# Performance work log

Hardware: AMD Instinct MI355X
Metric: run time of the kernel (lower is better)

The kernel has to match this reference:

```python
import jax, jax.numpy as jnp
import numpy as np

B, S, D, H, M = 4, 512, 768, 12, 4
DFF = 4 * D
HD = D // H
EPS = 1e-6  # timm/jvp_layers LayerNorm eps
SCALE = HD ** -0.5


def _ln(x, g, b):
    mu = jnp.mean(x, axis=-1, keepdims=True)
    var = jnp.mean((x - mu) ** 2, axis=-1, keepdims=True)
    return (x - mu) * jax.lax.rsqrt(var + EPS) * g + b


def _block(x, g1, b1, Wqkv, Wproj, bproj, g2, b2, W1, bf1, W2, bf2):
    # pre-norm attention
    h = _ln(x, g1, b1)
    qkv = h @ Wqkv                       # [B,S,3D]
    q, k, v = jnp.split(qkv, 3, axis=-1)
    q = q.reshape(B, S, H, HD)
    k = k.reshape(B, S, H, HD)
    v = v.reshape(B, S, H, HD)
    scores = jnp.einsum('bqhd,bkhd->bhqk', q, k) * SCALE
    attn = jax.nn.softmax(scores, axis=-1)
    o = jnp.einsum('bhqk,bkhd->bqhd', attn, v).reshape(B, S, D)
    x = x + o @ Wproj + bproj
    # pre-norm MLP
    h2 = _ln(x, g2, b2)
    mlp = jax.nn.gelu(h2 @ W1 + bf1, approximate=False) @ W2 + bf2
    return x + mlp


def setup_inputs() -> dict:
    key = jax.random.key(0)
    ks = jax.random.split(key, 8)
    w = 0.02
    return {
        'x': jax.random.normal(ks[0], (B, S, D), jnp.float32),
        'x_tangent': jax.random.normal(ks[1], (B, M, S, D), jnp.float32),
        'g1': jnp.ones((D,), jnp.float32),
        'b1': jnp.zeros((D,), jnp.float32),
        'Wqkv': jax.random.normal(ks[2], (D, 3 * D), jnp.float32) * w,
        'Wproj': jax.random.normal(ks[3], (D, D), jnp.float32) * w,
        'bproj': jnp.zeros((D,), jnp.float32),
        'g2': jnp.ones((D,), jnp.float32),
        'b2': jnp.zeros((D,), jnp.float32),
        'W1': jax.random.normal(ks[4], (D, DFF), jnp.float32) * w,
        'bf1': jnp.zeros((DFF,), jnp.float32),
        'W2': jax.random.normal(ks[5], (DFF, D), jnp.float32) * w,
        'bf2': jnp.zeros((D,), jnp.float32),
    }


def reference(x, x_tangent, g1, b1, Wqkv, Wproj, bproj, g2, b2, W1, bf1, W2, bf2):
    f = lambda xx: _block(xx, g1, b1, Wqkv, Wproj, bproj, g2, b2, W1, bf1, W2, bf2)
    # linearize once: primal + efficient JVP for all M tangent directions
    out, jvp_fn = jax.linearize(f, x)
    out_tangent = jax.vmap(jvp_fn, in_axes=1, out_axes=1)(x_tangent)  # [B,M,S,D]
    return out, out_tangent
```

## Files before the change

### kernel.cpp

```cpp
#include <hip/hip_runtime.h>
#include <math.h>

constexpr int B_ = 4, S_ = 512, D_ = 768, H_ = 12, M_ = 4, DFF_ = 3072, HD_ = 64;
constexpr float EPS_ = 1e-6f;
constexpr float SCALE_ = 0.125f;
constexpr int BS_ = B_ * S_;
constexpr int BH_ = B_ * H_;
constexpr long long BSD_ = (long long)BS_ * D_;
constexpr long long BS3D_ = (long long)BS_ * 3 * D_;
constexpr long long ATT_ = (long long)BH_ * S_ * S_;
constexpr long long BSF_ = (long long)BS_ * DFF_;

typedef __attribute__((ext_vector_type(8))) short bf16x8;
typedef __attribute__((ext_vector_type(4))) float f32x4;

__device__ __forceinline__ ushort f2bf(float f) {
    uint32_t u = __float_as_uint(f);
    u += 0x7FFF + ((u >> 16) & 1);
    return (ushort)(u >> 16);
}
__device__ __forceinline__ float bf2f(ushort u) {
    return __uint_as_float((uint32_t)u << 16);
}

__device__ __forceinline__ void gll16(const ushort* g, ushort* l) {
    __builtin_amdgcn_global_load_lds((const __attribute__((address_space(1))) void*)g,
                                     (__attribute__((address_space(3))) void*)l, 16, 0, 0);
}

template <int N> __device__ __forceinline__ void waitcnt_vm() {
    if constexpr (N == 0) asm volatile("s_waitcnt vmcnt(0)" ::: "memory");
    else if constexpr (N == 4) asm volatile("s_waitcnt vmcnt(4)" ::: "memory");
    else if constexpr (N == 6) asm volatile("s_waitcnt vmcnt(6)" ::: "memory");
    else if constexpr (N == 8) asm volatile("s_waitcnt vmcnt(8)" ::: "memory");
    else static_assert(N == 0 || N == 4 || N == 6 || N == 8, "add literal");
}

__device__ __forceinline__ void waitcnt_lgkm0() {
    asm volatile("s_waitcnt lgkmcnt(0)" ::: "memory");
    __builtin_amdgcn_sched_barrier(0);
}

__device__ __forceinline__ int xcd_swz(int flat, int nwg) {
    int q = nwg >> 3, r = nwg & 7;
    int x = flat & 7, pos = flat >> 3;
    int base = (x < r) ? x * (q + 1) : r * (q + 1) + (x - r) * q;
    return base + pos;
}

__device__ __forceinline__ size_t stroff(int rg, int c, int Nc) {
    int m = rg >> 11;
    int b = (rg >> 9) & (B_ - 1);
    int s = rg & (S_ - 1);
    return ((size_t)((b * M_ + m) * S_ + s)) * Nc + c;
}

__device__ __forceinline__ float block_sum(float v) {
    __shared__ float red[4];
    int tid = threadIdx.x;
#pragma unroll
    for (int off = 32; off > 0; off >>= 1) v += __shfl_down(v, off, 64);
    __syncthreads();
    if ((tid & 63) == 0) red[tid >> 6] = v;
    __syncthreads();
    return red[0] + red[1] + red[2] + red[3];
}

__device__ __forceinline__ float block_max(float v) {
    __shared__ float red[4];
    int tid = threadIdx.x;
#pragma unroll
    for (int off = 32; off > 0; off >>= 1) v = fmaxf(v, __shfl_down(v, off, 64));
    __syncthreads();
    if ((tid & 63) == 0) red[tid >> 6] = v;
    __syncthreads();
    return fmaxf(fmaxf(red[0], red[1]), fmaxf(red[2], red[3]));
}

__global__ __launch_bounds__(256) void transpose_f2b(const float* __restrict__ W,
                                                     ushort* __restrict__ WT,
                                                     int K, int N) {
    __shared__ float t[32][33];
    int n0 = blockIdx.x * 32, k0 = blockIdx.y * 32;
    int tx = threadIdx.x & 31, ty = threadIdx.x >> 5;
#pragma unroll
    for (int i = 0; i < 4; i++)
        t[ty + i * 8][tx] = W[(size_t)(k0 + ty + i * 8) * N + n0 + tx];
    __syncthreads();
#pragma unroll
    for (int i = 0; i < 4; i++)
        WT[(size_t)(n0 + ty + i * 8) * K + k0 + tx] = f2bf(t[tx][ty + i * 8]);
}

__global__ __launch_bounds__(256) void transpose_v(const ushort* __restrict__ src0,
                                                   ushort* __restrict__ Vt0,
                                                   ushort* __restrict__ dVt4) {
    int z = blockIdx.z;
    int m = z / BH_, bh = z % BH_;
    const ushort* qkvb = src0 + (size_t)m * BS3D_;
    ushort* Vt = (m == 0) ? Vt0 : dVt4 + (size_t)(m - 1) * BSD_;
    int b = bh / H_, hh = bh - b * H_;
    int s0 = blockIdx.x * 32, d0 = blockIdx.y * 32;
    __shared__ ushort t[32][33];
    int tx = threadIdx.x & 31, ty = threadIdx.x >> 5;
#pragma unroll
    for (int i = 0; i < 4; i++)
        t[ty + i * 8][tx] = qkvb[(size_t)(b * S_ + s0 + ty + i * 8) * 3 * D_ + 2 * D_ + hh * HD_ + d0 + tx];
    __syncthreads();
#pragma unroll
    for (int i = 0; i < 4; i++)
        Vt[(size_t)bh * HD_ * S_ + (size_t)(d0 + ty + i * 8) * S_ + s0 + tx] = t[tx][ty + i * 8];
}

__global__ __launch_bounds__(256) void ln_fwd(const float* __restrict__ xf,
                                              const ushort* __restrict__ xb,
                                              const float* __restrict__ g,
                                              const float* __restrict__ bta,
                                              ushort* __restrict__ xhat,
                                              ushort* __restrict__ h,
                                              float* __restrict__ rstd) {
    int row = blockIdx.x;
    size_t base = (size_t)row * D_;
    int tid = threadIdx.x;
    float v[3];
    float s = 0.f;
#pragma unroll
    for (int i = 0; i < 3; i++) {
        int c = tid + i * 256;
        v[i] = xf ? xf[base + c] : bf2f(xb[base + c]);
        s += v[i];
    }
    s = block_sum(s);
    float mu = s * (1.0f / D_);
    float vs = 0.f;
#pragma unroll
    for (int i = 0; i < 3; i++) { float c = v[i] - mu; vs += c * c; }
    vs = block_sum(vs);
    float rs = rsqrtf(vs * (1.0f / D_) + EPS_);
#pragma unroll
    for (int i = 0; i < 3; i++) {
        int c = tid + i * 256;
        float xh = (v[i] - mu) * rs;
        xhat[base + c] = f2bf(xh);
        h[base + c] = f2bf(xh * g[c] + bta[c]);
    }
    if (tid == 0) rstd[row] = rs;
}

__global__ __launch_bounds__(256) void ln_jvp(const float* __restrict__ tf,
                                              const ushort* __restrict__ tb, int mode,
                                              const ushort* __restrict__ xhat,
                                              const float* __restrict__ rstd,
                                              const float* __restrict__ g,
                                              ushort* __restrict__ dh,
                                              ushort* __restrict__ xtb) {
    int rg = blockIdx.x;
    int r = rg & (BS_ - 1);
    size_t pbase = (size_t)r * D_;
    int tid = threadIdx.x;
    float tv[3], xh[3];
    float s1 = 0.f, s2 = 0.f;
    size_t tbase;
    if (mode == 0) {
        int m = rg >> 11;
        int b = r >> 9, s = r & (S_ - 1);
        tbase = ((size_t)((b * M_ + m) * S_ + s)) * D_;
    } else {
        tbase = (size_t)rg * D_;
    }
#pragma unroll
    for (int i = 0; i < 3; i++) {
        int c = tid + i * 256;
        tv[i] = (mode == 0) ? tf[tbase + c] : bf2f(tb[tbase + c]);
        xh[i] = bf2f(xhat[pbase + c]);
        s1 += tv[i];
        s2 += tv[i] * xh[i];
    }
    s1 = block_sum(s1);
    s2 = block_sum(s2);
    float mt = s1 * (1.0f / D_);
    float mx = s2 * (1.0f / D_);
    float rs = rstd[r];
#pragma unroll
    for (int i = 0; i < 3; i++) {
        int c = tid + i * 256;
        dh[(size_t)rg * D_ + c] = f2bf(g[c] * rs * (tv[i] - mt - xh[i] * mx));
        if (mode == 0 && xtb) xtb[(size_t)rg * D_ + c] = f2bf(tv[i]);
    }
}

template <int BM, int BN, int EPI>
__global__ __launch_bounds__(256) void gemm_mfma(const ushort* __restrict__ A,
                                                 const ushort* __restrict__ BT,
                                                 const float* __restrict__ bias,
                                                 const float* __restrict__ resf,
                                                 const ushort* __restrict__ resb,
                                                 const ushort* __restrict__ resb2,
                                                 float* __restrict__ Cf,
                                                 float* __restrict__ Cf2,
                                                 ushort* __restrict__ Cb,
                                                 ushort* __restrict__ aux,
                                                 int Nc, int Kd) {
    constexpr int FI = BM / 32, FJ = BN / 32;
    constexpr int LA = BM / 32, LB = BN / 32, L = LA + LB;
    __shared__ ushort As[2][BM * 64];
    __shared__ ushort Bs[2][BN * 64];
    int tid = threadIdx.x;
    int wave = tid >> 6, lane = tid & 63;
    int wr = wave >> 1, wc = wave & 1;
    int gx = gridDim.x, nwg = gx * gridDim.y;
    int work = xcd_swz(blockIdx.x + blockIdx.y * gx, nwg);
    int band = work / (8 * gx);
    int wi = work - band * (8 * gx);
    int row0 = (band * 8 + (wi & 7)) * BM;
    int col0 = (wi >> 3) * BN;

    int srow = lane >> 3;
    int skel = ((lane & 7) ^ (lane >> 3)) * 8;
    const ushort* Ag0 = A + (size_t)(row0 + srow) * Kd + skel;
    const ushort* Bg0 = BT + (size_t)(col0 + srow) * Kd + skel;

    auto stage = [&](int bufi, int k0) {
#pragma unroll
        for (int cc = 0; cc < LA; cc++) {
            int c = wave * LA + cc;
            gll16(Ag0 + (size_t)(c * 8) * Kd + k0, As[bufi] + c * 512);
        }
#pragma unroll
        for (int cc = 0; cc < LB; cc++) {
            int c = wave * LB + cc;
            gll16(Bg0 + (size_t)(c * 8) * Kd + k0, Bs[bufi] + c * 512);
        }
    };

    int frow = lane & 15, fkb = (lane >> 4) * 8;
    int aoff[2][FI], boff[2][FJ];
#pragma unroll
    for (int ks = 0; ks < 2; ks++) {
        int sw = (fkb + ks * 32) ^ ((frow & 7) * 8);
#pragma unroll
        for (int i = 0; i < FI; i++) aoff[ks][i] = (wr * (BM / 2) + i * 16 + frow) * 64 + sw;
#pragma unroll
        for (int j = 0; j < FJ; j++) boff[ks][j] = (wc * (BN / 2) + j * 16 + frow) * 64 + sw;
    }

    f32x4 acc[FI][FJ] = {};

    int nt = Kd >> 6;
    stage(0, 0);
    if (nt > 1) { stage(1, 64); waitcnt_vm<L>(); }
    else        { waitcnt_vm<0>(); }
    __builtin_amdgcn_s_barrier();
    __builtin_amdgcn_sched_barrier(0);

    int cur = 0;
    for (int t = 0; t < nt; t++) {
        bf16x8 af[2][FI], bfv[2][FJ];
        const ushort* Ab = As[cur];
        const ushort* Bb = Bs[cur];
#pragma unroll
        for (int ks = 0; ks < 2; ks++) {
#pragma unroll
            for (int i = 0; i < FI; i++) af[ks][i] = *(const bf16x8*)(Ab + aoff[ks][i]);
#pragma unroll
            for (int j = 0; j < FJ; j++) bfv[ks][j] = *(const bf16x8*)(Bb + boff[ks][j]);
        }
        waitcnt_lgkm0();
        __builtin_amdgcn_s_barrier();
        if (t + 2 < nt) {
            stage(cur, (t + 2) << 6);
            __builtin_amdgcn_sched_barrier(0);
        }
#pragma unroll
        for (int ks = 0; ks < 2; ks++)
#pragma unroll
            for (int i = 0; i < FI; i++)
#pragma unroll
                for (int j = 0; j < FJ; j++)
                    acc[i][j] = __builtin_amdgcn_mfma_f32_16x16x32_bf16(af[ks][i], bfv[ks][j], acc[i][j], 0, 0, 0);
        __builtin_amdgcn_sched_barrier(0);
        if (t + 2 < nt) waitcnt_vm<L>();
        else if (t + 1 < nt) waitcnt_vm<0>();
        __builtin_amdgcn_s_barrier();
        __builtin_amdgcn_sched_barrier(0);
        cur ^= 1;
    }

#pragma unroll
    for (int i = 0; i < FI; i++) {
        int rbase = row0 + wr * (BM / 2) + i * 16 + (lane >> 4) * 4;
#pragma unroll
        for (int j = 0; j < FJ; j++) {
            int c = col0 + wc * (BN / 2) + j * 16 + (lane & 15);
#pragma unroll
            for (int r = 0; r < 4; r++) {
                int rg = rbase + r;
                size_t off = (size_t)rg * Nc + c;
                float v = acc[i][j][r];
                if (EPI == 0) {
                    Cb[off] = f2bf(v);
                } else if (EPI == 1) {
                    v += bias[c];
                    float cdf = 0.5f * (1.0f + erff(v * 0.70710678118654752f));
                    Cb[off] = f2bf(v * cdf);
                    aux[off] = f2bf(cdf + v * 0.39894228040143267f * expf(-0.5f * v * v));
                } else if (EPI == 2) {
                    Cb[off] = f2bf(v * bf2f(aux[(size_t)(rg & (BS_ - 1)) * Nc + c]));
                } else if (EPI == 4) {
                    v += bias[c] + bf2f(resb[off]);
                    Cf[off] = v;
                } else if (EPI == 5) {
                    if (rg < BS_) {
                        v += bias[c] + resf[off];
                        Cb[off] = f2bf(v);
                    } else {
                        int rg2 = rg - BS_;
                        v += bf2f(resb[(size_t)rg2 * Nc + c]);
                        aux[(size_t)rg2 * Nc + c] = f2bf(v);
                    }
                } else {
                    v += bf2f(resb2[(size_t)rg * Nc + c]);
                    Cf2[stroff(rg, c, Nc)] = v;
                }
            }
        }
    }
}

template <bool TAN>
__global__ __launch_bounds__(256) void attn_qk_mfma(const ushort* __restrict__ qkvb,
                                                    const ushort* __restrict__ dqkvp,
                                                    ushort* __restrict__ sc) {
    int work = xcd_swz(blockIdx.x, gridDim.x);
    constexpr int NT = S_ / 128;
    int mz = work / (BH_ * NT * NT);
    int rem = work % (BH_ * NT * NT);
    int bh = rem / (NT * NT);
    int r2 = rem % (NT * NT);
    int q0 = (r2 / NT) * 128, kc0 = (r2 % NT) * 128;
    int b = bh / H_, hh = bh - b * H_;
    const size_t qoff = (size_t)b * S_ * 3 * D_ + hh * HD_;
    const int ld = 3 * D_;
    const ushort* dqkv = TAN ? dqkvp + (size_t)mz * BS3D_ : nullptr;
    __shared__ ushort As[128 * 64];
    __shared__ ushort Bs[128 * 64];
    __shared__ ushort dAs[TAN ? 128 * 64 : 1];
    __shared__ ushort dBs[TAN ? 128 * 64 : 1];
    int tid = threadIdx.x;
    int wave = tid >> 6, lane = tid & 63;
    int wr = wave >> 1, wc = wave & 1;

    int srow = lane >> 3;
    int skel = ((lane & 7) ^ (lane >> 3)) * 8;
    const ushort* Ag0 = qkvb + qoff + (size_t)(q0 + srow) * ld + skel;
    const ushort* Bg0 = qkvb + qoff + D_ + (size_t)(kc0 + srow) * ld + skel;

#pragma unroll
    for (int cc = 0; cc < 4; cc++) {
        int c = wave * 4 + cc;
        gll16(Ag0 + (size_t)(c * 8) * ld, As + c * 512);
        gll16(Bg0 + (size_t)(c * 8) * ld, Bs + c * 512);
        if (TAN) {
            gll16(dqkv + qoff + (size_t)(q0 + c * 8 + srow) * ld + skel, dAs + c * 512);
            gll16(dqkv + qoff + D_ + (size_t)(kc0 + c * 8 + srow) * ld + skel, dBs + c * 512);
        }
    }
    __syncthreads();

    int frow = lane & 15, fkb = (lane >> 4) * 8;
    f32x4 acc[4][4] = {};
#pragma unroll
    for (int ks = 0; ks < 2; ks++) {
        int sw = (fkb + ks * 32) ^ ((frow & 7) * 8);
        bf16x8 af[4], bfv[4];
#pragma unroll
        for (int i = 0; i < 4; i++) af[i] = *(const bf16x8*)(As + (wr * 64 + i * 16 + frow) * 64 + sw);
#pragma unroll
        for (int j = 0; j < 4; j++) bfv[j] = *(const bf16x8*)(Bs + (wc * 64 + j * 16 + frow) * 64 + sw);
        if (!TAN) {
#pragma unroll
            for (int i = 0; i < 4; i++)
#pragma unroll
                for (int j = 0; j < 4; j++)
                    acc[i][j] = __builtin_amdgcn_mfma_f32_16x16x32_bf16(af[i], bfv[j], acc[i][j], 0, 0, 0);
        } else {
            bf16x8 daf[4], dbf[4];
#pragma unroll
            for (int i = 0; i < 4; i++) daf[i] = *(const bf16x8*)(dAs + (wr * 64 + i * 16 + frow) * 64 + sw);
#pragma unroll
            for (int j = 0; j < 4; j++) dbf[j] = *(const bf16x8*)(dBs + (wc * 64 + j * 16 + frow) * 64 + sw);
#pragma unroll
            for (int i = 0; i < 4; i++)
#pragma unroll
                for (int j = 0; j < 4; j++) {
                    acc[i][j] = __builtin_amdgcn_mfma_f32_16x16x32_bf16(daf[i], bfv[j], acc[i][j], 0, 0, 0);
                    acc[i][j] = __builtin_amdgcn_mfma_f32_16x16x32_bf16(af[i], dbf[j], acc[i][j], 0, 0, 0);
                }
        }
    }

    ushort* scm = sc + (size_t)mz * ATT_;
#pragma unroll
    for (int i = 0; i < 4; i++) {
        int rbase = q0 + wr * 64 + i * 16 + (lane >> 4) * 4;
#pragma unroll
        for (int j = 0; j < 4; j++) {
            int c = kc0 + wc * 64 + j * 16 + (lane & 15);
#pragma unroll
            for (int r = 0; r < 4; r++)
                scm[((size_t)bh * S_ + rbase + r) * S_ + c] = f2bf(acc[i][j][r] * SCALE_);
        }
    }
}

__global__ __launch_bounds__(256) void attn_av_p(const ushort* __restrict__ Pb,
                                                 const ushort* __restrict__ Vt,
                                                 ushort* __restrict__ outp) {
    int work = xcd_swz(blockIdx.x, gridDim.x);
    constexpr int NT = S_ / 128;
    int bh = work / NT;
    int q0 = (work % NT) * 128;
    int b = bh / H_, hh = bh - b * H_;
    const ushort* Pg = Pb + (size_t)bh * S_ * S_;
    const ushort* Vg = Vt + (size_t)bh * HD_ * S_;
    __shared__ ushort As[128 * 64];
    __shared__ ushort Bs[64 * 64];
    int tid = threadIdx.x;
    int wave = tid >> 6, lane = tid & 63;
    int wr = wave >> 1, wc = wave & 1;
    int srow = lane >> 3;
    int skel = ((lane & 7) ^ (lane >> 3)) * 8;
    int frow = lane & 15, fkb = (lane >> 4) * 8;

    f32x4 acc[4][2] = {};
    for (int k0 = 0; k0 < S_; k0 += 64) {
#pragma unroll
        for (int cc = 0; cc < 4; cc++) {
            int c = wave * 4 + cc;
            gll16(Pg + (size_t)(q0 + c * 8 + srow) * S_ + k0 + skel, As + c * 512);
        }
#pragma unroll
        for (int cc = 0; cc < 2; cc++) {
            int c = wave * 2 + cc;
            gll16(Vg + (size_t)(c * 8 + srow) * S_ + k0 + skel, Bs + c * 512);
        }
        __syncthreads();
#pragma unroll
        for (int ks = 0; ks < 2; ks++) {
            int sw = (fkb + ks * 32) ^ ((frow & 7) * 8);
            bf16x8 af[4], bfv[2];
#pragma unroll
            for (int i = 0; i < 4; i++) af[i] = *(const bf16x8*)(As + (wr * 64 + i * 16 + frow) * 64 + sw);
#pragma unroll
            for (int j = 0; j < 2; j++) bfv[j] = *(const bf16x8*)(Bs + (wc * 32 + j * 16 + frow) * 64 + sw);
#pragma unroll
            for (int i = 0; i < 4; i++)
#pragma unroll
                for (int j = 0; j < 2; j++)
                    acc[i][j] = __builtin_amdgcn_mfma_f32_16x16x32_bf16(af[i], bfv[j], acc[i][j], 0, 0, 0);
        }
        __syncthreads();
    }

#pragma unroll
    for (int i = 0; i < 4; i++) {
        int rbase = q0 + wr * 64 + i * 16 + (lane >> 4) * 4;
#pragma unroll
        for (int j = 0; j < 2; j++) {
            int c = hh * HD_ + wc * 32 + j * 16 + (lane & 15);
#pragma unroll
            for (int r = 0; r < 4; r++)
                outp[(size_t)(b * S_ + rbase + r) * D_ + c] = f2bf(acc[i][j][r]);
        }
    }
}

__global__ __launch_bounds__(256) void attn_av_tan(const ushort* __restrict__ Pb,
                                                   const ushort* __restrict__ dscp,
                                                   const ushort* __restrict__ Vt,
                                                   const ushort* __restrict__ dVtp,
                                                   const ushort* __restrict__ Ob,
                                                   ushort* __restrict__ outp) {
    int work = xcd_swz(blockIdx.x, gridDim.x);
    int mz = work / (BH_ * 4);
    int rem = work % (BH_ * 4);
    int bh = rem / 4;
    int q0 = (rem % 4) * 128;
    int b = bh / H_, hh = bh - b * H_;
    const ushort* Pg = Pb + (size_t)bh * S_ * S_;
    const ushort* Dg = dscp + (size_t)mz * ATT_ + (size_t)bh * S_ * S_;
    const ushort* Vg = Vt + (size_t)bh * HD_ * S_;
    const ushort* dVg = dVtp + (size_t)mz * BSD_ + (size_t)bh * HD_ * S_;
    ushort* outm = outp + (size_t)mz * BSD_;
    __shared__ ushort Ps[128 * 64], Ds[128 * 64], Vs[64 * 64], dVs[64 * 64];
    int tid = threadIdx.x;
    int wave = tid >> 6, lane = tid & 63;
    int wr = wave >> 1, wc = wave & 1;
    int srow = lane >> 3;
    int skel = ((lane & 7) ^ (lane >> 3)) * 8;
    int frow = lane & 15, fkb = (lane >> 4) * 8;
    int aoff[2][4], boff[2][2];
#pragma unroll
    for (int ks = 0; ks < 2; ks++) {
        int sw = (fkb + ks * 32) ^ ((frow & 7) * 8);
#pragma unroll
        for (int i = 0; i < 4; i++) aoff[ks][i] = (wr * 64 + i * 16 + frow) * 64 + sw;
#pragma unroll
        for (int j = 0; j < 2; j++) boff[ks][j] = (wc * 32 + j * 16 + frow) * 64 + sw;
    }

    float s[4] = {0.f, 0.f, 0.f, 0.f};
    f32x4 acc[4][2] = {};

    for (int k0 = 0; k0 < S_; k0 += 64) {
#pragma unroll
        for (int cc = 0; cc < 4; cc++) {
            int c = wave * 4 + cc;
            gll16(Pg + (size_t)(q0 + c * 8 + srow) * S_ + k0 + skel, Ps + c * 512);
            gll16(Dg + (size_t)(q0 + c * 8 + srow) * S_ + k0 + skel, Ds + c * 512);
        }
#pragma unroll
        for (int cc = 0; cc < 2; cc++) {
            int c = wave * 2 + cc;
            gll16(Vg + (size_t)(c * 8 + srow) * S_ + k0 + skel, Vs + c * 512);
            gll16(dVg + (size_t)(c * 8 + srow) * S_ + k0 + skel, dVs + c * 512);
        }
        __syncthreads();
#pragma unroll
        for (int ks = 0; ks < 2; ks++) {
            bf16x8 p8[4], pq8[4], v8[2], dv8[2];
#pragma unroll
            for (int i = 0; i < 4; i++) {
                p8[i] = *(const bf16x8*)(Ps + aoff[ks][i]);
                bf16x8 d8 = *(const bf16x8*)(Ds + aoff[ks][i]);
#pragma unroll
                for (int e = 0; e < 8; e++) {
                    float pd = bf2f((ushort)p8[i][e]) * bf2f((ushort)d8[e]);
                    s[i] += pd;
                    pq8[i][e] = (short)f2bf(pd);
                }
            }
#pragma unroll
            for (int j = 0; j < 2; j++) {
                v8[j] = *(const bf16x8*)(Vs + boff[ks][j]);
                dv8[j] = *(const bf16x8*)(dVs + boff[ks][j]);
            }
#pragma unroll
            for (int i = 0; i < 4; i++)
#pragma unroll
                for (int j = 0; j < 2; j++) {
                    acc[i][j] = __builtin_amdgcn_mfma_f32_16x16x32_bf16(pq8[i], v8[j], acc[i][j], 0, 0, 0);
                    acc[i][j] = __builtin_amdgcn_mfma_f32_16x16x32_bf16(p8[i], dv8[j], acc[i][j], 0, 0, 0);
                }
        }
        __syncthreads();
    }

#pragma unroll
    for (int i = 0; i < 4; i++) {
        s[i] += __shfl_xor(s[i], 16);
        s[i] += __shfl_xor(s[i], 32);
    }

#pragma unroll
    for (int i = 0; i < 4; i++) {
        int rbase = q0 + wr * 64 + i * 16 + (lane >> 4) * 4;
#pragma unroll
        for (int r = 0; r < 4; r++) {
            float sc = __shfl(s[i], ((lane >> 4) << 2) + r);
#pragma unroll
            for (int j = 0; j < 2; j++) {
                int c = hh * HD_ + wc * 32 + j * 16 + (lane & 15);
                float o = bf2f(Ob[(size_t)(b * S_ + rbase + r) * D_ + c]);
                outm[(size_t)(b * S_ + rbase + r) * D_ + c] = f2bf(acc[i][j][r] - sc * o);
            }
        }
    }
}

__global__ __launch_bounds__(256) void softmax_rows(const ushort* __restrict__ sc,
                                                    ushort* __restrict__ scb) {
    size_t row = blockIdx.x;
    const ushort* p = sc + row * S_;
    int tid = threadIdx.x;
    ushort2 vu = *(const ushort2*)&p[tid * 2];
    float v0 = bf2f(vu.x), v1 = bf2f(vu.y);
    float mx = block_max(fmaxf(v0, v1));
    float e0 = expf(v0 - mx), e1 = expf(v1 - mx);
    float s = block_sum(e0 + e1);
    float inv = 1.0f / s;
    ushort2 ob; ob.x = f2bf(e0 * inv); ob.y = f2bf(e1 * inv);
    *(ushort2*)&scb[row * S_ + tid * 2] = ob;
}

extern "C" void kernel_launch(void* const* d_in, const int* in_sizes, int n_in,
                              void* d_out, int out_size, void* d_ws, size_t ws_size,
                              hipStream_t stream) {
    const float* x = (const float*)d_in[0];
    const float* xt = (const float*)d_in[1];
    const float* g1 = (const float*)d_in[2];
    const float* b1 = (const float*)d_in[3];
    const float* Wqkv = (const float*)d_in[4];
    const float* Wproj = (const float*)d_in[5];
    const float* bproj = (const float*)d_in[6];
    const float* g2 = (const float*)d_in[7];
    const float* b2 = (const float*)d_in[8];
    const float* W1 = (const float*)d_in[9];
    const float* bf1 = (const float*)d_in[10];
    const float* W2 = (const float*)d_in[11];
    const float* bf2 = (const float*)d_in[12];
    float* out = (float*)d_out;
    float* out_t = out + BSD_;

    char* wp = (char*)d_ws;
    auto alloc = [&](size_t bytes) { void* p = wp; wp += (bytes + 255) & ~(size_t)255; return p; };
    char* regBig = (char*)alloc(25 * BSD_ * 2);
    ushort* hb5 = (ushort*)regBig;
    ushort* ob5 = (ushort*)(regBig + 5 * BSD_ * 2);
    ushort* qkv5 = (ushort*)(regBig + 10 * BSD_ * 2);
    ushort* ab5 = (ushort*)regBig;
    ushort* xhat1 = (ushort*)alloc(BSD_ * 2);
    ushort* x2b = xhat1;
    ushort* xhat2 = (ushort*)alloc(BSD_ * 2);
    ushort* h2b = (ushort*)alloc(BSD_ * 2);
    ushort* dx2b = (ushort*)alloc(4 * BSD_ * 2);
    ushort* xt_b = (ushort*)alloc(4 * BSD_ * 2);
    ushort* Vt = (ushort*)alloc(BSD_ * 2);
    ushort* dscb2 = (ushort*)alloc(2 * ATT_ * 2);
    ushort* attnb = (ushort*)alloc(ATT_ * 2);
    ushort* gpb = (ushort*)alloc(BSF_ * 2);
    ushort* dh2_4 = (ushort*)alloc(4 * BSD_ * 2);
    ushort* dVt4 = (ushort*)alloc(4 * BSD_ * 2);
    float* rstd1 = (float*)alloc(BS_ * 4);
    float* rstd2 = (float*)alloc(BS_ * 4);
    ushort* WqkvT = (ushort*)alloc((size_t)D_ * 3 * D_ * 2);
    ushort* WprojT = (ushort*)alloc((size_t)D_ * D_ * 2);
    ushort* W1T = (ushort*)alloc((size_t)DFF_ * D_ * 2);
    ushort* W2T = (ushort*)alloc((size_t)D_ * DFF_ * 2);

    transpose_f2b<<<dim3(3 * D_ / 32, D_ / 32), 256, 0, stream>>>(Wqkv, WqkvT, D_, 3 * D_);
    transpose_f2b<<<dim3(D_ / 32, D_ / 32), 256, 0, stream>>>(Wproj, WprojT, D_, D_);
    transpose_f2b<<<dim3(DFF_ / 32, D_ / 32), 256, 0, stream>>>(W1, W1T, D_, DFF_);
    transpose_f2b<<<dim3(D_ / 32, DFF_ / 32), 256, 0, stream>>>(W2, W2T, DFF_, D_);

    ln_fwd<<<BS_, 256, 0, stream>>>(x, nullptr, g1, b1, xhat1, hb5, rstd1);
    ln_jvp<<<4 * BS_, 256, 0, stream>>>(xt, nullptr, 0, xhat1, rstd1, g1, hb5 + BSD_, xt_b);
    gemm_mfma<128, 128, 0><<<dim3(3 * D_ / 128, 5 * BS_ / 128), 256, 0, stream>>>(
        hb5, WqkvT, nullptr, nullptr, nullptr, nullptr, nullptr, nullptr, qkv5, nullptr, 3 * D_, D_);
    transpose_v<<<dim3(S_ / 32, HD_ / 32, 5 * BH_), 256, 0, stream>>>(qkv5, Vt, dVt4);

    attn_qk_mfma<false><<<(S_ / 128) * (S_ / 128) * BH_, 256, 0, stream>>>(qkv5, nullptr, dscb2);
    softmax_rows<<<BH_ * S_, 256, 0, stream>>>(dscb2, attnb);
    attn_av_p<<<(S_ / 128) * BH_, 256, 0, stream>>>(attnb, Vt, ob5);

    const ushort* dqkv4 = qkv5 + BS3D_;
    for (int p = 0; p < 2; p++) {
        attn_qk_mfma<true><<<2 * (S_ / 128) * (S_ / 128) * BH_, 256, 0, stream>>>(
            qkv5, dqkv4 + (size_t)p * 2 * BS3D_, dscb2);
        attn_av_tan<<<2 * 4 * BH_, 256, 0, stream>>>(
            attnb, dscb2, Vt, dVt4 + (size_t)p * 2 * BSD_, ob5, ob5 + BSD_ + (size_t)p * 2 * BSD_);
    }

    gemm_mfma<128, 64, 5><<<dim3(D_ / 64, 5 * BS_ / 128), 256, 0, stream>>>(
        ob5, WprojT, bproj, x, xt_b, nullptr, nullptr, nullptr, x2b, dx2b, D_, D_);

    ln_fwd<<<BS_, 256, 0, stream>>>(nullptr, x2b, g2, b2, xhat2, h2b, rstd2);
    gemm_mfma<128, 128, 1><<<dim3(DFF_ / 128, BS_ / 128), 256, 0, stream>>>(
        h2b, W1T, bf1, nullptr, nullptr, nullptr, nullptr, nullptr, ab5, gpb, DFF_, D_);
    ln_jvp<<<4 * BS_, 256, 0, stream>>>(nullptr, dx2b, 1, xhat2, rstd2, g2, dh2_4, nullptr);
    gemm_mfma<128, 128, 2><<<dim3(DFF_ / 128, 4 * BS_ / 128), 256, 0, stream>>>(
        dh2_4, W1T, nullptr, nullptr, nullptr, nullptr, nullptr, nullptr, ab5 + BSF_, gpb, DFF_, D_);

    gemm_mfma<64, 64, 4><<<dim3(D_ / 64, BS_ / 64), 256, 0, stream>>>(
        ab5, W2T, bf2, nullptr, x2b, nullptr, out, nullptr, nullptr, nullptr, D_, DFF_);
    gemm_mfma<128, 64, 6><<<dim3(D_ / 64, 4 * BS_ / 128), 256, 0, stream>>>(
        ab5 + BSF_, W2T, nullptr, nullptr, nullptr, dx2b, nullptr, out_t, nullptr, nullptr, D_, DFF_);
}
```

Measured before the change: 428.5 us.

## Fuse tangent score computation into tangent attention-value kernel

Tangent attention scores (dQ·K + Q·dK) are now computed per 64-key tile inside the tangent A·V kernel and staged in shared memory, instead of being written to and read back from a global bf16 score buffer. All four tangent directions run in one launch with 64-row query tiles, replacing two pairs of launches. This removes the global write and read of the tangent score matrices and shrinks the workspace. In exchange each block reloads K and dK per tile, adds an extra barrier per iteration, and uses smaller tiles, which lowers MFMA density per block.

```diff
diff --git a/kernel.cpp b/kernel.cpp
--- a/kernel.cpp
+++ b/kernel.cpp
@@ -327,25 +327,18 @@
     }
 }
 
-template <bool TAN>
 __global__ __launch_bounds__(256) void attn_qk_mfma(const ushort* __restrict__ qkvb,
-                                                    const ushort* __restrict__ dqkvp,
                                                     ushort* __restrict__ sc) {
     int work = xcd_swz(blockIdx.x, gridDim.x);
     constexpr int NT = S_ / 128;
-    int mz = work / (BH_ * NT * NT);
-    int rem = work % (BH_ * NT * NT);
-    int bh = rem / (NT * NT);
-    int r2 = rem % (NT * NT);
+    int bh = work / (NT * NT);
+    int r2 = work % (NT * NT);
     int q0 = (r2 / NT) * 128, kc0 = (r2 % NT) * 128;
     int b = bh / H_, hh = bh - b * H_;
     const size_t qoff = (size_t)b * S_ * 3 * D_ + hh * HD_;
     const int ld = 3 * D_;
-    const ushort* dqkv = TAN ? dqkvp + (size_t)mz * BS3D_ : nullptr;
     __shared__ ushort As[128 * 64];
     __shared__ ushort Bs[128 * 64];
-    __shared__ ushort dAs[TAN ? 128 * 64 : 1];
-    __shared__ ushort dBs[TAN ? 128 * 64 : 1];
     int tid = threadIdx.x;
     int wave = tid >> 6, lane = tid & 63;
     int wr = wave >> 1, wc = wave & 1;
@@ -360,10 +353,6 @@
         int c = wave * 4 + cc;
         gll16(Ag0 + (size_t)(c * 8) * ld, As + c * 512);
         gll16(Bg0 + (size_t)(c * 8) * ld, Bs + c * 512);
-        if (TAN) {
-            gll16(dqkv + qoff + (size_t)(q0 + c * 8 + srow) * ld + skel, dAs + c * 512);
-            gll16(dqkv + qoff + D_ + (size_t)(kc0 + c * 8 + srow) * ld + skel, dBs + c * 512);
-        }
     }
     __syncthreads();
 
@@ -377,29 +366,13 @@
         for (int i = 0; i < 4; i++) af[i] = *(const bf16x8*)(As + (wr * 64 + i * 16 + frow) * 64 + sw);
 #pragma unroll
         for (int j = 0; j < 4; j++) bfv[j] = *(const bf16x8*)(Bs + (wc * 64 + j * 16 + frow) * 64 + sw);
-        if (!TAN) {
-#pragma unroll
-            for (int i = 0; i < 4; i++)
-#pragma unroll
-                for (int j = 0; j < 4; j++)
-                    acc[i][j] = __builtin_amdgcn_mfma_f32_16x16x32_bf16(af[i], bfv[j], acc[i][j], 0, 0, 0);
-        } else {
-            bf16x8 daf[4], dbf[4];
-#pragma unroll
-            for (int i = 0; i < 4; i++) daf[i] = *(const bf16x8*)(dAs + (wr * 64 + i * 16 + frow) * 64 + sw);
-#pragma unroll
-            for (int j = 0; j < 4; j++) dbf[j] = *(const bf16x8*)(dBs + (wc * 64 + j * 16 + frow) * 64 + sw);
-#pragma unroll
-            for (int i = 0; i < 4; i++)
-#pragma unroll
-                for (int j = 0; j < 4; j++) {
-                    acc[i][j] = __builtin_amdgcn_mfma_f32_16x16x32_bf16(daf[i], bfv[j], acc[i][j], 0, 0, 0);
-                    acc[i][j] = __builtin_amdgcn_mfma_f32_16x16x32_bf16(af[i], dbf[j], acc[i][j], 0, 0, 0);
-                }
-        }
-    }
-
-    ushort* scm = sc + (size_t)mz * ATT_;
+#pragma unroll
+        for (int i = 0; i < 4; i++)
+#pragma unroll
+            for (int j = 0; j < 4; j++)
+                acc[i][j] = __builtin_amdgcn_mfma_f32_16x16x32_bf16(af[i], bfv[j], acc[i][j], 0, 0, 0);
+    }
+
 #pragma unroll
     for (int i = 0; i < 4; i++) {
         int rbase = q0 + wr * 64 + i * 16 + (lane >> 4) * 4;
@@ -408,7 +381,7 @@
             int c = kc0 + wc * 64 + j * 16 + (lane & 15);
 #pragma unroll
             for (int r = 0; r < 4; r++)
-                scm[((size_t)bh * S_ + rbase + r) * S_ + c] = f2bf(acc[i][j][r] * SCALE_);
+                sc[((size_t)bh * S_ + rbase + r) * S_ + c] = f2bf(acc[i][j][r] * SCALE_);
         }
     }
 }
@@ -475,62 +448,115 @@
     }
 }
 
-__global__ __launch_bounds__(256) void attn_av_tan(const ushort* __restrict__ Pb,
-                                                   const ushort* __restrict__ dscp,
-                                                   const ushort* __restrict__ Vt,
-                                                   const ushort* __restrict__ dVtp,
-                                                   const ushort* __restrict__ Ob,
-                                                   ushort* __restrict__ outp) {
+__global__ __launch_bounds__(256) void attn_tan_fused(const ushort* __restrict__ qkv5,
+                                                      const ushort* __restrict__ Pb,
+                                                      const ushort* __restrict__ Vt,
+                                                      const ushort* __restrict__ dVt4,
+                                                      const ushort* __restrict__ Ob,
+                                                      ushort* __restrict__ outp) {
     int work = xcd_swz(blockIdx.x, gridDim.x);
-    int mz = work / (BH_ * 4);
-    int rem = work % (BH_ * 4);
-    int bh = rem / 4;
-    int q0 = (rem % 4) * 128;
+    int mz = work / (BH_ * 8);
+    int rem = work % (BH_ * 8);
+    int bh = rem / 8;
+    int q0 = (rem % 8) * 64;
     int b = bh / H_, hh = bh - b * H_;
+    const int ld = 3 * D_;
+    const size_t qoff = (size_t)b * S_ * 3 * D_ + hh * HD_;
+    const ushort* Qg = qkv5 + qoff;
+    const ushort* Kg = qkv5 + qoff + D_;
+    const ushort* dQg = qkv5 + (size_t)(1 + mz) * BS3D_ + qoff;
+    const ushort* dKg = dQg + D_;
+    const ushort* Vg = Vt + (size_t)bh * HD_ * S_;
+    const ushort* dVg = dVt4 + (size_t)mz * BSD_ + (size_t)bh * HD_ * S_;
     const ushort* Pg = Pb + (size_t)bh * S_ * S_;
-    const ushort* Dg = dscp + (size_t)mz * ATT_ + (size_t)bh * S_ * S_;
-    const ushort* Vg = Vt + (size_t)bh * HD_ * S_;
-    const ushort* dVg = dVtp + (size_t)mz * BSD_ + (size_t)bh * HD_ * S_;
     ushort* outm = outp + (size_t)mz * BSD_;
-    __shared__ ushort Ps[128 * 64], Ds[128 * 64], Vs[64 * 64], dVs[64 * 64];
+
+    __shared__ ushort Qs[64 * 64], dQs[64 * 64];
+    __shared__ ushort Ks[64 * 64], dKs[64 * 64];
+    __shared__ ushort Vs[64 * 64], dVs[64 * 64];
+    __shared__ ushort Ps[64 * 64], Ds[64 * 64];
+
     int tid = threadIdx.x;
     int wave = tid >> 6, lane = tid & 63;
     int wr = wave >> 1, wc = wave & 1;
     int srow = lane >> 3;
     int skel = ((lane & 7) ^ (lane >> 3)) * 8;
     int frow = lane & 15, fkb = (lane >> 4) * 8;
-    int aoff[2][4], boff[2][2];
+
+    int aoff[2][2], boff[2][2];
 #pragma unroll
     for (int ks = 0; ks < 2; ks++) {
         int sw = (fkb + ks * 32) ^ ((frow & 7) * 8);
 #pragma unroll
-        for (int i = 0; i < 4; i++) aoff[ks][i] = (wr * 64 + i * 16 + frow) * 64 + sw;
+        for (int i = 0; i < 2; i++) aoff[ks][i] = (wr * 32 + i * 16 + frow) * 64 + sw;
 #pragma unroll
         for (int j = 0; j < 2; j++) boff[ks][j] = (wc * 32 + j * 16 + frow) * 64 + sw;
     }
 
-    float s[4] = {0.f, 0.f, 0.f, 0.f};
-    f32x4 acc[4][2] = {};
+#pragma unroll
+    for (int cc = 0; cc < 2; cc++) {
+        int c = wave * 2 + cc;
+        gll16(Qg + (size_t)(q0 + c * 8 + srow) * ld + skel, Qs + c * 512);
+        gll16(dQg + (size_t)(q0 + c * 8 + srow) * ld + skel, dQs + c * 512);
+    }
+
+    float s[2] = {0.f, 0.f};
+    f32x4 acc[2][2] = {};
 
     for (int k0 = 0; k0 < S_; k0 += 64) {
-#pragma unroll
-        for (int cc = 0; cc < 4; cc++) {
-            int c = wave * 4 + cc;
-            gll16(Pg + (size_t)(q0 + c * 8 + srow) * S_ + k0 + skel, Ps + c * 512);
-            gll16(Dg + (size_t)(q0 + c * 8 + srow) * S_ + k0 + skel, Ds + c * 512);
-        }
 #pragma unroll
         for (int cc = 0; cc < 2; cc++) {
             int c = wave * 2 + cc;
+            gll16(Kg + (size_t)(k0 + c * 8 + srow) * ld + skel, Ks + c * 512);
+            gll16(dKg + (size_t)(k0 + c * 8 + srow) * ld + skel, dKs + c * 512);
             gll16(Vg + (size_t)(c * 8 + srow) * S_ + k0 + skel, Vs + c * 512);
             gll16(dVg + (size_t)(c * 8 + srow) * S_ + k0 + skel, dVs + c * 512);
+            gll16(Pg + (size_t)(q0 + c * 8 + srow) * S_ + k0 + skel, Ps + c * 512);
         }
         __syncthreads();
+
+        f32x4 accd[2][2] = {};
 #pragma unroll
         for (int ks = 0; ks < 2; ks++) {
-            bf16x8 p8[4], pq8[4], v8[2], dv8[2];
-#pragma unroll
-            for (int i = 0; i < 4; i++) {
+            bf16x8 aq[2], adq[2], bk[2], bdk[2];
+#pragma unroll
+            for (int i = 0; i < 2; i++) {
+                aq[i] = *(const bf16x8*)(Qs + aoff[ks][i]);
+                adq[i] = *(const bf16x8*)(dQs + aoff[ks][i]);
+            }
+#pragma unroll
+            for (int j = 0; j < 2; j++) {
+                bk[j] = *(const bf16x8*)(Ks + boff[ks][j]);
+                bdk[j] = *(const bf16x8*)(dKs + boff[ks][j]);
+            }
+#pragma unroll
+            for (int i = 0; i < 2; i++)
+#pragma unroll
+                for (int j = 0; j < 2; j++) {
+                    accd[i][j] = __builtin_amdgcn_mfma_f32_16x16x32_bf16(adq[i], bk[j], accd[i][j], 0, 0, 0);
+                    accd[i][j] = __builtin_amdgcn_mfma_f32_16x16x32_bf16(aq[i], bdk[j], accd[i][j], 0, 0, 0);
+                }
+        }
+#pragma unroll
+        for (int i = 0; i < 2; i++) {
+#pragma unroll
+            for (int j = 0; j < 2; j++) {
+#pragma unroll
+                for (int r = 0; r < 4; r++) {
+                    int qq = wr * 32 + i * 16 + (lane >> 4) * 4 + r;
+                    int kk = wc * 32 + j * 16 + (lane & 15);
+                    int blk = ((kk >> 3) ^ (qq & 7));
+                    Ds[qq * 64 + blk * 8 + (kk & 7)] = f2bf(accd[i][j][r] * SCALE_);
+                }
+            }
+        }
+        __syncthreads();
+
+#pragma unroll
+        for (int ks = 0; ks < 2; ks++) {
+            bf16x8 p8[2], pq8[2], v8[2], dv8[2];
+#pragma unroll
+            for (int i = 0; i < 2; i++) {
                 p8[i] = *(const bf16x8*)(Ps + aoff[ks][i]);
                 bf16x8 d8 = *(const bf16x8*)(Ds + aoff[ks][i]);
 #pragma unroll
@@ -546,7 +572,7 @@
                 dv8[j] = *(const bf16x8*)(dVs + boff[ks][j]);
             }
 #pragma unroll
-            for (int i = 0; i < 4; i++)
+            for (int i = 0; i < 2; i++)
 #pragma unroll
                 for (int j = 0; j < 2; j++) {
                     acc[i][j] = __builtin_amdgcn_mfma_f32_16x16x32_bf16(pq8[i], v8[j], acc[i][j], 0, 0, 0);
@@ -557,14 +583,14 @@
     }
 
 #pragma unroll
-    for (int i = 0; i < 4; i++) {
+    for (int i = 0; i < 2; i++) {
         s[i] += __shfl_xor(s[i], 16);
         s[i] += __shfl_xor(s[i], 32);
     }
 
 #pragma unroll
-    for (int i = 0; i < 4; i++) {
-        int rbase = q0 + wr * 64 + i * 16 + (lane >> 4) * 4;
+    for (int i = 0; i < 2; i++) {
+        int rbase = q0 + wr * 32 + i * 16 + (lane >> 4) * 4;
 #pragma unroll
         for (int r = 0; r < 4; r++) {
             float sc = __shfl(s[i], ((lane >> 4) << 2) + r);
@@ -626,7 +652,7 @@
     ushort* dx2b = (ushort*)alloc(4 * BSD_ * 2);
     ushort* xt_b = (ushort*)alloc(4 * BSD_ * 2);
     ushort* Vt = (ushort*)alloc(BSD_ * 2);
-    ushort* dscb2 = (ushort*)alloc(2 * ATT_ * 2);
+    ushort* scb = (ushort*)alloc(ATT_ * 2);
     ushort* attnb = (ushort*)alloc(ATT_ * 2);
     ushort* gpb = (ushort*)alloc(BSF_ * 2);
     ushort* dh2_4 = (ushort*)alloc(4 * BSD_ * 2);
@@ -649,17 +675,11 @@
         hb5, WqkvT, nullptr, nullptr, nullptr, nullptr, nullptr, nullptr, qkv5, nullptr, 3 * D_, D_);
     transpose_v<<<dim3(S_ / 32, HD_ / 32, 5 * BH_), 256, 0, stream>>>(qkv5, Vt, dVt4);
 
-    attn_qk_mfma<false><<<(S_ / 128) * (S_ / 128) * BH_, 256, 0, stream>>>(qkv5, nullptr, dscb2);
-    softmax_rows<<<BH_ * S_, 256, 0, stream>>>(dscb2, attnb);
+    attn_qk_mfma<<<(S_ / 128) * (S_ / 128) * BH_, 256, 0, stream>>>(qkv5, scb);
+    softmax_rows<<<BH_ * S_, 256, 0, stream>>>(scb, attnb);
     attn_av_p<<<(S_ / 128) * BH_, 256, 0, stream>>>(attnb, Vt, ob5);
 
-    const ushort* dqkv4 = qkv5 + BS3D_;
-    for (int p = 0; p < 2; p++) {
-        attn_qk_mfma<true><<<2 * (S_ / 128) * (S_ / 128) * BH_, 256, 0, stream>>>(
-            qkv5, dqkv4 + (size_t)p * 2 * BS3D_, dscb2);
-        attn_av_tan<<<2 * 4 * BH_, 256, 0, stream>>>(
-            attnb, dscb2, Vt, dVt4 + (size_t)p * 2 * BSD_, ob5, ob5 + BSD_ + (size_t)p * 2 * BSD_);
-    }
+    attn_tan_fused<<<4 * 8 * BH_, 256, 0, stream>>>(qkv5, attnb, Vt, dVt4, ob5, ob5 + BSD_);
 
     gemm_mfma<128, 64, 5><<<dim3(D_ / 64, 5 * BS_ / 128), 256, 0, stream>>>(
         ob5, WprojT, bproj, x, xt_b, nullptr, nullptr, nullptr, x2b, dx2b, D_, D_);
```

Measured after the change: 392.1 us. 1.09x faster.
